# Kernel optimization log

Measured on AMD Instinct MI355X. Metric: run time of the kernel, lower is better.

Reference implementation:

```python
import jax, jax.numpy as jnp
import numpy as np

DIM = 2048
NUM_HEADS = 16
HEAD_DIM = 128
INNER = NUM_HEADS * HEAD_DIM


def rotate_half(x):
    x1, x2 = jnp.split(x, 2, axis=-1)
    return jnp.concatenate([-x2, x1], axis=-1)


def rope_tables(T, head_dim):
    inv_freq = 1.0 / (10000.0 ** (np.arange(0, head_dim, 2, dtype=np.float32) / head_dim))
    t = np.arange(T, dtype=np.float32)
    freqs = np.einsum('i,j->ij', t, inv_freq)  # [T, hd/2]
    emb = np.concatenate([freqs, freqs], axis=-1)  # [T, hd]
    return jnp.asarray(np.cos(emb)), jnp.asarray(np.sin(emb))


def setup_inputs() -> dict:
    key = jax.random.key(0)
    k1, k2, k3 = jax.random.split(key, 3)
    B, T = 2, 2048
    x = jax.random.normal(k1, (B, T, DIM), dtype=jnp.float32)
    scale = 1.0 / np.sqrt(DIM)
    w_qkv = jax.random.normal(k2, (DIM, 3 * INNER), dtype=jnp.float32) * scale
    w_out = jax.random.normal(k3, (INNER, DIM), dtype=jnp.float32) * (1.0 / np.sqrt(INNER))
    return {"x": x, "w_qkv": w_qkv, "w_out": w_out}


def reference(x, w_qkv, w_out):
    B, T, _ = x.shape
    qkv = x @ w_qkv  # [B, T, 3*INNER]
    q, k, v = jnp.split(qkv, 3, axis=-1)
    # [B, H, T, hd]
    q = q.reshape(B, T, NUM_HEADS, HEAD_DIM).transpose(0, 2, 1, 3)
    k = k.reshape(B, T, NUM_HEADS, HEAD_DIM).transpose(0, 2, 1, 3)
    v = v.reshape(B, T, NUM_HEADS, HEAD_DIM).transpose(0, 2, 1, 3)
    cos, sin = rope_tables(T, HEAD_DIM)  # [T, hd]
    cos = cos[None, None]
    sin = sin[None, None]
    q = q * cos + rotate_half(q) * sin
    k = k * cos + rotate_half(k) * sin
    # causal SDPA
    scale = 1.0 / np.sqrt(HEAD_DIM)
    scores = jnp.einsum('bhqd,bhkd->bhqk', q, k) * scale
    mask = jnp.tril(jnp.ones((T, T), dtype=bool))
    scores = jnp.where(mask[None, None], scores, jnp.finfo(scores.dtype).min)
    attn = jax.nn.softmax(scores, axis=-1)
    out = jnp.einsum('bhqk,bhkd->bhqd', attn, v)
    out = out.transpose(0, 2, 1, 3).reshape(B, T, INNER)
    return out @ w_out
```

## Files before the change

### kernel.cpp

```cpp
#include <hip/hip_runtime.h>
#include <hip/hip_bf16.h>
#include <math.h>

typedef __bf16 bf16x8 __attribute__((ext_vector_type(8)));
typedef float f32x4 __attribute__((ext_vector_type(4)));
typedef float f32x16 __attribute__((ext_vector_type(16)));
typedef unsigned short ushort8_t __attribute__((ext_vector_type(8)));
typedef unsigned short ushort4_t __attribute__((ext_vector_type(4)));

#define DIMSZ 2048
#define NHEADS 16
#define HD 128
#define INNER 2048
#define T_SEQ 2048
#define BATCH 2
#define BT_ROWS (BATCH * T_SEQ)
#define QKV_COLS (3 * INNER)

__device__ __forceinline__ float bf2f(unsigned short u) {
  union { unsigned int ui; float f; } v; v.ui = ((unsigned int)u) << 16; return v.f;
}
__device__ __forceinline__ unsigned short f2bf(float f) {
  union { float f; unsigned int ui; } v; v.f = f;
  unsigned int u = v.ui;
  return (unsigned short)((u + 0x7FFFu + ((u >> 16) & 1u)) >> 16);
}
__device__ __forceinline__ bf16x8 ld8(const unsigned short* p) {
  return *(const bf16x8*)p;
}
__device__ __forceinline__ void gl16(const unsigned short* g, unsigned short* l) {
  __builtin_amdgcn_global_load_lds(
      (const __attribute__((address_space(1))) unsigned int*)g,
      (__attribute__((address_space(3))) unsigned int*)l, 16, 0, 0);
}

__global__ void detect_dtype(const unsigned short* __restrict__ w, int* __restrict__ flag) {
  __shared__ int sh;
  if (threadIdx.x == 0) sh = 0;
  __syncthreads();
  int hit = 0;
  for (int i = threadIdx.x; i < 8192; i += 256) {
    unsigned int e = (w[i] >> 7) & 0xFF;
    if (e >= 0x7F) hit = 1;
  }
  if (hit) atomicOr(&sh, 1);
  __syncthreads();
  if (threadIdx.x == 0) *flag = sh;
}

__global__ void convert_x(const void* __restrict__ in, unsigned short* __restrict__ out,
                          const int* __restrict__ flag) {
  const bool f32 = (*flag != 0);
  size_t i = ((size_t)blockIdx.x * 256 + threadIdx.x) * 8;
  if (f32) {
    const float* inf = (const float*)in;
    float4 u0 = *(const float4*)&inf[i];
    float4 u1 = *(const float4*)&inf[i + 4];
    ushort8_t t;
    t[0] = f2bf(u0.x); t[1] = f2bf(u0.y); t[2] = f2bf(u0.z); t[3] = f2bf(u0.w);
    t[4] = f2bf(u1.x); t[5] = f2bf(u1.y); t[6] = f2bf(u1.z); t[7] = f2bf(u1.w);
    *(ushort8_t*)&out[i] = t;
  } else {
    *(uint4*)&out[i] = *(const uint4*)&((const unsigned short*)in)[i];
  }
}

__global__ void transpose_any(const void* __restrict__ in, unsigned short* __restrict__ out,
                              int R, int C, const int* __restrict__ flag) {
  const bool f32 = (*flag != 0);
  __shared__ unsigned short tile[32][33];
  int c0 = blockIdx.x * 32, r0 = blockIdx.y * 32;
  int tx = threadIdx.x & 31, ty = threadIdx.x >> 5;
  if (f32) {
    const float* inf = (const float*)in;
    #pragma unroll
    for (int i = 0; i < 4; ++i)
      tile[ty + i * 8][tx] = f2bf(inf[(size_t)(r0 + ty + i * 8) * C + c0 + tx]);
  } else {
    const unsigned short* inu = (const unsigned short*)in;
    #pragma unroll
    for (int i = 0; i < 4; ++i)
      tile[ty + i * 8][tx] = inu[(size_t)(r0 + ty + i * 8) * C + c0 + tx];
  }
  __syncthreads();
  #pragma unroll
  for (int i = 0; i < 4; ++i)
    out[(size_t)(c0 + ty + i * 8) * R + r0 + tx] = tile[tx][ty + i * 8];
}

__global__ __launch_bounds__(256) void gemm_lds(const unsigned short* __restrict__ A,
                                                const unsigned short* __restrict__ Bt,
                                                unsigned short* __restrict__ Cb,
                                                float* __restrict__ Cf,
                                                int M, int N, int K) {
  __shared__ unsigned short As[128 * 32];
  __shared__ unsigned short Bs[128 * 32];
  const int tid = threadIdx.x;
  const int m0 = blockIdx.y * 128, n0 = blockIdx.x * 128;
  const int w = tid >> 6, L = tid & 63, lane = tid & 63, c = lane & 15, quad = lane >> 4;
  const int wm = (w & 1) * 64, wn = (w >> 1) * 64;
  f32x4 acc[4][4];
  #pragma unroll
  for (int i = 0; i < 4; ++i)
    #pragma unroll
    for (int j = 0; j < 4; ++j) acc[i][j] = (f32x4)0.0f;

  for (int k0 = 0; k0 < K; k0 += 32) {
    #pragma unroll
    for (int p = 0; p < 2; ++p) {
      int ci = p * 256 + w * 64 + L;
      int r = ci >> 2, s = ci & 3;
      gl16(&A[(size_t)(m0 + r) * K + k0 + s * 8], &As[(size_t)(p * 256 + w * 64) * 8]);
      gl16(&Bt[(size_t)(n0 + r) * K + k0 + s * 8], &Bs[(size_t)(p * 256 + w * 64) * 8]);
    }
    __syncthreads();
    bf16x8 af[4], bfr[4];
    #pragma unroll
    for (int i = 0; i < 4; ++i) af[i] = ld8(&As[(wm + i * 16 + c) * 32 + quad * 8]);
    #pragma unroll
    for (int j = 0; j < 4; ++j) bfr[j] = ld8(&Bs[(wn + j * 16 + c) * 32 + quad * 8]);
    #pragma unroll
    for (int i = 0; i < 4; ++i)
      #pragma unroll
      for (int j = 0; j < 4; ++j)
        acc[i][j] = __builtin_amdgcn_mfma_f32_16x16x32_bf16(af[i], bfr[j], acc[i][j], 0, 0, 0);
    __syncthreads();
  }
  if (Cf) {
    #pragma unroll
    for (int i = 0; i < 4; ++i)
      #pragma unroll
      for (int j = 0; j < 4; ++j)
        #pragma unroll
        for (int r = 0; r < 4; ++r)
          Cf[(size_t)(m0 + wm + i * 16 + quad * 4 + r) * N + n0 + wn + j * 16 + c] = acc[i][j][r];
  } else {
    #pragma unroll
    for (int i = 0; i < 4; ++i)
      #pragma unroll
      for (int j = 0; j < 4; ++j)
        #pragma unroll
        for (int r = 0; r < 4; ++r)
          Cb[(size_t)(m0 + wm + i * 16 + quad * 4 + r) * N + n0 + wn + j * 16 + c] =
              f2bf(acc[i][j][r]);
  }
}

__global__ void rope_kernel(unsigned short* __restrict__ qkv) {
  int idx = blockIdx.x * 256 + threadIdx.x;
  int jb = (idx & 7) * 8;
  int head = (idx >> 3) & 15;
  int qk = (idx >> 7) & 1;
  int row = idx >> 8;
  int t = row & (T_SEQ - 1);
  size_t base = (size_t)row * QKV_COLS + qk * INNER + head * HD + jb;
  ushort8_t x1 = *(ushort8_t*)&qkv[base];
  ushort8_t x2 = *(ushort8_t*)&qkv[base + 64];
  ushort8_t o1, o2;
  #pragma unroll
  for (int e = 0; e < 8; ++e) {
    float inv_freq = exp2f(-(float)(jb + e) * 0.20762050593046017f);
    float ang = (float)t * inv_freq;
    float sn = sinf(ang), cs = cosf(ang);
    float a = bf2f(x1[e]), bq = bf2f(x2[e]);
    o1[e] = f2bf(a * cs - bq * sn);
    o2[e] = f2bf(bq * cs + a * sn);
  }
  *(ushort8_t*)&qkv[base] = o1;
  *(ushort8_t*)&qkv[base + 64] = o2;
}

#define KT3 64
#define KSTR3 136
#define VSTR3 72
#define PSTR3 68
#define SM_VS (64 * KSTR3 * 2)
#define SM_PS (SM_VS + 128 * VSTR3 * 2)
#define SM_LR (SM_PS + 64 * PSTR3 * 2)
#define SM_TOT (SM_LR + 2 * 64 * 4)
__global__ __launch_bounds__(256, 2) void flash_attn3(const unsigned short* __restrict__ qkv,
                                                      unsigned short* __restrict__ aout) {
  __shared__ char smem[SM_TOT];
  unsigned short* Ks = (unsigned short*)smem;
  unsigned short* Vs = (unsigned short*)(smem + SM_VS);
  unsigned short* Ps = (unsigned short*)(smem + SM_PS);
  float* lred = (float*)(smem + SM_LR);
  float* Os = (float*)smem;

  const int tid = threadIdx.x, wave = tid >> 6, lane = tid & 63;
  const int wq = wave & 1, wk = wave >> 1;
  const int l31 = lane & 31, lh = lane >> 5;
  const int bh = blockIdx.y, b = bh >> 4, h = bh & 15;
  const unsigned short* qbase = qkv + (size_t)b * T_SEQ * QKV_COLS + h * HD;
  const unsigned short* kbase = qbase + INNER;
  const unsigned short* vbase = qbase + 2 * INNER;
  const float cf = 0.12751743f;

  for (int half = 0; half < 2; ++half) {
    const int qt = (half == 0) ? (int)blockIdx.x : 31 - (int)blockIdx.x;
    const int q0 = qt * 64;
    const int qg = q0 + wq * 32 + l31;

    bf16x8 aq[8];
    #pragma unroll
    for (int ch = 0; ch < 8; ++ch)
      aq[ch] = ld8(&qbase[(size_t)qg * QKV_COLS + ch * 16 + lh * 8]);

    f32x16 o[4];
    #pragma unroll
    for (int dt = 0; dt < 4; ++dt) o[dt] = (f32x16)0.0f;
    float l_part = 0.0f;

    const int nkt = qt + 1;
    for (int it = 0; it < nkt; ++it) {
      const int kt = it * KT3;
      __syncthreads();
      #pragma unroll
      for (int p = 0; p < 4; ++p) {
        int ci = p * 256 + tid, r = ci >> 4, s = ci & 15;
        *(uint4*)&Ks[r * KSTR3 + s * 8] = *(const uint4*)&kbase[(size_t)(kt + r) * QKV_COLS + s * 8];
      }
      {
        int rp = tid & 31, seg = tid >> 5;
        const unsigned short* vp = &vbase[(size_t)(kt + 2 * rp) * QKV_COLS + seg * 16];
        ushort8_t v0a = *(const ushort8_t*)vp;
        ushort8_t v0b = *(const ushort8_t*)(vp + 8);
        ushort8_t v1a = *(const ushort8_t*)(vp + QKV_COLS);
        ushort8_t v1b = *(const ushort8_t*)(vp + QKV_COLS + 8);
        #pragma unroll
        for (int e = 0; e < 8; ++e) {
          *(unsigned int*)&Vs[(seg * 16 + e) * VSTR3 + 2 * rp] =
              (unsigned int)v0a[e] | ((unsigned int)v1a[e] << 16);
          *(unsigned int*)&Vs[(seg * 16 + 8 + e) * VSTR3 + 2 * rp] =
              (unsigned int)v0b[e] | ((unsigned int)v1b[e] << 16);
        }
      }
      __syncthreads();

      f32x16 st = (f32x16)0.0f;
      #pragma unroll
      for (int ch = 0; ch < 8; ++ch) {
        bf16x8 kf = ld8(&Ks[(wk * 32 + l31) * KSTR3 + ch * 16 + lh * 8]);
        st = __builtin_amdgcn_mfma_f32_32x32x16_bf16(kf, aq[ch], st, 0, 0, 0);
      }
      unsigned short* prow = &Ps[(wq * 32 + l31) * PSTR3 + wk * 32];
      #pragma unroll
      for (int g = 0; g < 4; ++g) {
        ushort4_t pk;
        #pragma unroll
        for (int e = 0; e < 4; ++e) {
          int r = g * 4 + e;
          int keyl = e + 8 * g + 4 * lh;
          int kg = kt + wk * 32 + keyl;
          float p = (kg <= qg) ? exp2f(st[r] * cf) : 0.0f;
          l_part += p;
          pk[e] = f2bf(p);
        }
        *(ushort4_t*)&prow[g * 8 + 4 * lh] = pk;
      }
      bf16x8 pf[2];
      #pragma unroll
      for (int kc = 0; kc < 2; ++kc) {
        uint2 pa = *(const uint2*)&Ps[(wq * 32 + l31) * PSTR3 + wk * 32 + kc * 16 + lh * 8];
        uint2 pb = *(const uint2*)&Ps[(wq * 32 + l31) * PSTR3 + wk * 32 + kc * 16 + lh * 8 + 4];
        union { uint4 u; bf16x8 v; } cvt;
        cvt.u.x = pa.x; cvt.u.y = pa.y; cvt.u.z = pb.x; cvt.u.w = pb.y;
        pf[kc] = cvt.v;
      }
      #pragma unroll
      for (int dt = 0; dt < 4; ++dt) {
        #pragma unroll
        for (int kc = 0; kc < 2; ++kc) {
          bf16x8 vf = ld8(&Vs[(dt * 32 + l31) * VSTR3 + wk * 32 + kc * 16 + lh * 8]);
          o[dt] = __builtin_amdgcn_mfma_f32_32x32x16_bf16(pf[kc], vf, o[dt], 0, 0, 0);
        }
      }
    }

    float lv = l_part + __shfl_xor(l_part, 32, 64);
    __syncthreads();
    if (lane < 32) lred[wk * 64 + wq * 32 + lane] = lv;
    if (wk == 1) {
      #pragma unroll
      for (int dt = 0; dt < 4; ++dt)
        #pragma unroll
        for (int s = 0; s < 4; ++s) {
          f32x4 seg4 = {o[dt][s * 4 + 0], o[dt][s * 4 + 1], o[dt][s * 4 + 2], o[dt][s * 4 + 3]};
          *(f32x4*)&Os[(size_t)(wq * 64 + lane) * 68 + dt * 16 + s * 4] = seg4;
        }
    }
    __syncthreads();
    if (wk == 0) {
      float invr[16];
      #pragma unroll
      for (int r = 0; r < 16; ++r) {
        int ql = wq * 32 + (r & 3) + 8 * (r >> 2) + 4 * lh;
        invr[r] = 1.0f / (lred[ql] + lred[64 + ql]);
      }
      #pragma unroll
      for (int dt = 0; dt < 4; ++dt) {
        f32x4 add[4];
        #pragma unroll
        for (int s = 0; s < 4; ++s)
          add[s] = *(const f32x4*)&Os[(size_t)(wq * 64 + lane) * 68 + dt * 16 + s * 4];
        #pragma unroll
        for (int r = 0; r < 16; ++r) {
          float val = (o[dt][r] + add[r >> 2][r & 3]) * invr[r];
          int qrow = q0 + wq * 32 + (r & 3) + 8 * (r >> 2) + 4 * lh;
          aout[(size_t)((size_t)b * T_SEQ + qrow) * INNER + h * HD + dt * 32 + l31] = f2bf(val);
        }
      }
    }
  }
}

extern "C" void kernel_launch(void* const* d_in, const int* in_sizes, int n_in,
                              void* d_out, int out_size, void* d_ws, size_t ws_size,
                              hipStream_t stream) {
  const void* x     = d_in[0];
  const void* w_qkv = d_in[1];
  const void* w_out = d_in[2];
  float* out = (float*)d_out;

  int* flag = (int*)d_ws;
  unsigned short* qkvbuf  = (unsigned short*)((char*)d_ws + 256);
  unsigned short* attnout = qkvbuf + (size_t)BT_ROWS * QKV_COLS;
  unsigned short* wqkvT   = attnout + (size_t)BT_ROWS * INNER;
  unsigned short* woutT   = wqkvT + (size_t)QKV_COLS * DIMSZ;
  unsigned short* xb      = woutT + (size_t)DIMSZ * INNER;

  detect_dtype<<<1, 256, 0, stream>>>((const unsigned short*)w_qkv, flag);
  convert_x<<<dim3((size_t)BT_ROWS * DIMSZ / 2048), 256, 0, stream>>>(x, xb, flag);
  transpose_any<<<dim3(QKV_COLS / 32, DIMSZ / 32), 256, 0, stream>>>(w_qkv, wqkvT, DIMSZ, QKV_COLS, flag);
  transpose_any<<<dim3(DIMSZ / 32, INNER / 32), 256, 0, stream>>>(w_out, woutT, INNER, DIMSZ, flag);
  gemm_lds<<<dim3(QKV_COLS / 128, BT_ROWS / 128), 256, 0, stream>>>(xb, wqkvT, qkvbuf, nullptr, BT_ROWS, QKV_COLS, DIMSZ);
  rope_kernel<<<dim3(BT_ROWS * NHEADS * 2 * 8 / 256), 256, 0, stream>>>(qkvbuf);
  flash_attn3<<<dim3(16, BATCH * NHEADS), 256, 0, stream>>>(qkvbuf, attnout);
  gemm_lds<<<dim3(DIMSZ / 128, BT_ROWS / 128), 256, 0, stream>>>(attnout, woutT, nullptr, out, BT_ROWS, DIMSZ, INNER);
}
```

Baseline: 451.6 us.

## Fuse RoPE into QKV GEMM epilogue, widen K tile with swizzle, prefetch KV

The QKV projection now applies rotary embedding in its epilogue, reading precomputed cos/sin tables that a small kernel fills once per call, so the separate rope kernel and its full read/write of Q and K are gone. The GEMM K-step is widened from 32 to 64 with an XOR-swizzled LDS layout to reduce bank conflicts and halve barrier count. The attention kernel now prefetches the next K/V tile into registers while the current tile is being computed. The costs are higher register and LDS use, and the tables are stored in the attention-output buffer, which is safe only because they are consumed before attention writes that buffer.

```diff
diff --git a/kernel.cpp b/kernel.cpp
--- a/kernel.cpp
+++ b/kernel.cpp
@@ -88,16 +88,33 @@
     out[(size_t)(c0 + ty + i * 8) * R + r0 + tx] = tile[tx][ty + i * 8];
 }
 
-__global__ __launch_bounds__(256) void gemm_lds(const unsigned short* __restrict__ A,
-                                                const unsigned short* __restrict__ Bt,
-                                                unsigned short* __restrict__ Cb,
-                                                float* __restrict__ Cf,
-                                                int M, int N, int K) {
-  __shared__ unsigned short As[128 * 32];
-  __shared__ unsigned short Bs[128 * 32];
+__global__ void rope_tables(float* __restrict__ ct, float* __restrict__ st) {
+  int i = blockIdx.x * 256 + threadIdx.x;
+  int t = i >> 6, j = i & 63;
+  float inv_freq = exp2f(-(float)j * 0.20762050593046017f);
+  float ang = (float)t * inv_freq;
+  ct[i] = cosf(ang);
+  st[i] = sinf(ang);
+}
+
+#define GBK 64
+__global__ __launch_bounds__(256) void gemm_lds2(const unsigned short* __restrict__ A,
+                                                 const unsigned short* __restrict__ Bt,
+                                                 unsigned short* __restrict__ Cb,
+                                                 float* __restrict__ Cf,
+                                                 int M, int N, int K,
+                                                 const float* __restrict__ costab,
+                                                 const float* __restrict__ sintab,
+                                                 int rope_limit) {
+  __shared__ union {
+    unsigned short stage[2][128 * GBK];
+    unsigned short tile[128 * 136];
+  } sm;
+  unsigned short* As = sm.stage[0];
+  unsigned short* Bs = sm.stage[1];
   const int tid = threadIdx.x;
   const int m0 = blockIdx.y * 128, n0 = blockIdx.x * 128;
-  const int w = tid >> 6, L = tid & 63, lane = tid & 63, c = lane & 15, quad = lane >> 4;
+  const int w = tid >> 6, L = tid & 63, c = L & 15, quad = L >> 4;
   const int wm = (w & 1) * 64, wn = (w >> 1) * 64;
   f32x4 acc[4][4];
   #pragma unroll
@@ -105,25 +122,31 @@
     #pragma unroll
     for (int j = 0; j < 4; ++j) acc[i][j] = (f32x4)0.0f;
 
-  for (int k0 = 0; k0 < K; k0 += 32) {
-    #pragma unroll
-    for (int p = 0; p < 2; ++p) {
+  for (int k0 = 0; k0 < K; k0 += GBK) {
+    #pragma unroll
+    for (int p = 0; p < 4; ++p) {
       int ci = p * 256 + w * 64 + L;
-      int r = ci >> 2, s = ci & 3;
-      gl16(&A[(size_t)(m0 + r) * K + k0 + s * 8], &As[(size_t)(p * 256 + w * 64) * 8]);
-      gl16(&Bt[(size_t)(n0 + r) * K + k0 + s * 8], &Bs[(size_t)(p * 256 + w * 64) * 8]);
-    }
-    __syncthreads();
-    bf16x8 af[4], bfr[4];
-    #pragma unroll
-    for (int i = 0; i < 4; ++i) af[i] = ld8(&As[(wm + i * 16 + c) * 32 + quad * 8]);
-    #pragma unroll
-    for (int j = 0; j < 4; ++j) bfr[j] = ld8(&Bs[(wn + j * 16 + c) * 32 + quad * 8]);
-    #pragma unroll
-    for (int i = 0; i < 4; ++i)
+      int r = ci >> 3, s = ci & 7;
+      int sl = s ^ (r & 7);
+      gl16(&A[(size_t)(m0 + r) * K + k0 + sl * 8], &As[(p * 256 + w * 64) * 8]);
+      gl16(&Bt[(size_t)(n0 + r) * K + k0 + sl * 8], &Bs[(p * 256 + w * 64) * 8]);
+    }
+    __syncthreads();
+    #pragma unroll
+    for (int sub = 0; sub < 2; ++sub) {
+      bf16x8 af[4], bfr[4];
+      #pragma unroll
+      for (int i = 0; i < 4; ++i)
+        af[i] = ld8(&As[(wm + i * 16 + c) * GBK + (((sub * 4 + quad) ^ (c & 7)) * 8)]);
       #pragma unroll
       for (int j = 0; j < 4; ++j)
-        acc[i][j] = __builtin_amdgcn_mfma_f32_16x16x32_bf16(af[i], bfr[j], acc[i][j], 0, 0, 0);
+        bfr[j] = ld8(&Bs[(wn + j * 16 + c) * GBK + (((sub * 4 + quad) ^ (c & 7)) * 8)]);
+      #pragma unroll
+      for (int i = 0; i < 4; ++i)
+        #pragma unroll
+        for (int j = 0; j < 4; ++j)
+          acc[i][j] = __builtin_amdgcn_mfma_f32_16x16x32_bf16(af[i], bfr[j], acc[i][j], 0, 0, 0);
+    }
     __syncthreads();
   }
   if (Cf) {
@@ -134,6 +157,40 @@
         #pragma unroll
         for (int r = 0; r < 4; ++r)
           Cf[(size_t)(m0 + wm + i * 16 + quad * 4 + r) * N + n0 + wn + j * 16 + c] = acc[i][j][r];
+  } else if (n0 < rope_limit) {
+    #pragma unroll
+    for (int i = 0; i < 4; ++i)
+      #pragma unroll
+      for (int j = 0; j < 4; ++j)
+        #pragma unroll
+        for (int r = 0; r < 4; ++r)
+          sm.tile[(wm + i * 16 + quad * 4 + r) * 136 + wn + j * 16 + c] = f2bf(acc[i][j][r]);
+    __syncthreads();
+    int rbase = w * 8 + (L >> 3);
+    int cb = (L & 7) * 8;
+    #pragma unroll
+    for (int p = 0; p < 4; ++p) {
+      int row = rbase + p * 32;
+      int tp = (m0 + row) & (T_SEQ - 1);
+      const float* cr = &costab[tp * 64 + cb];
+      const float* sr = &sintab[tp * 64 + cb];
+      float4 c0v = *(const float4*)cr, c1v = *(const float4*)(cr + 4);
+      float4 s0v = *(const float4*)sr, s1v = *(const float4*)(sr + 4);
+      float cv[8] = {c0v.x, c0v.y, c0v.z, c0v.w, c1v.x, c1v.y, c1v.z, c1v.w};
+      float sv[8] = {s0v.x, s0v.y, s0v.z, s0v.w, s1v.x, s1v.y, s1v.z, s1v.w};
+      bf16x8 x1 = ld8(&sm.tile[row * 136 + cb]);
+      bf16x8 x2 = ld8(&sm.tile[row * 136 + cb + 64]);
+      ushort8_t o1, o2;
+      #pragma unroll
+      for (int e = 0; e < 8; ++e) {
+        float a = (float)x1[e], bq = (float)x2[e];
+        o1[e] = f2bf(a * cv[e] - bq * sv[e]);
+        o2[e] = f2bf(bq * cv[e] + a * sv[e]);
+      }
+      *(ushort8_t*)&Cb[(size_t)(m0 + row) * N + n0 + cb] = o1;
+      *(ushort8_t*)&Cb[(size_t)(m0 + row) * N + n0 + cb + 64] = o2;
+    }
+    __syncthreads();
   } else {
     #pragma unroll
     for (int i = 0; i < 4; ++i)
@@ -144,30 +201,6 @@
           Cb[(size_t)(m0 + wm + i * 16 + quad * 4 + r) * N + n0 + wn + j * 16 + c] =
               f2bf(acc[i][j][r]);
   }
-}
-
-__global__ void rope_kernel(unsigned short* __restrict__ qkv) {
-  int idx = blockIdx.x * 256 + threadIdx.x;
-  int jb = (idx & 7) * 8;
-  int head = (idx >> 3) & 15;
-  int qk = (idx >> 7) & 1;
-  int row = idx >> 8;
-  int t = row & (T_SEQ - 1);
-  size_t base = (size_t)row * QKV_COLS + qk * INNER + head * HD + jb;
-  ushort8_t x1 = *(ushort8_t*)&qkv[base];
-  ushort8_t x2 = *(ushort8_t*)&qkv[base + 64];
-  ushort8_t o1, o2;
-  #pragma unroll
-  for (int e = 0; e < 8; ++e) {
-    float inv_freq = exp2f(-(float)(jb + e) * 0.20762050593046017f);
-    float ang = (float)t * inv_freq;
-    float sn = sinf(ang), cs = cosf(ang);
-    float a = bf2f(x1[e]), bq = bf2f(x2[e]);
-    o1[e] = f2bf(a * cs - bq * sn);
-    o2[e] = f2bf(bq * cs + a * sn);
-  }
-  *(ushort8_t*)&qkv[base] = o1;
-  *(ushort8_t*)&qkv[base + 64] = o2;
 }
 
 #define KT3 64
@@ -178,7 +211,7 @@
 #define SM_PS (SM_VS + 128 * VSTR3 * 2)
 #define SM_LR (SM_PS + 64 * PSTR3 * 2)
 #define SM_TOT (SM_LR + 2 * 64 * 4)
-__global__ __launch_bounds__(256, 2) void flash_attn3(const unsigned short* __restrict__ qkv,
+__global__ __launch_bounds__(256, 2) void flash_attn4(const unsigned short* __restrict__ qkv,
                                                       unsigned short* __restrict__ aout) {
   __shared__ char smem[SM_TOT];
   unsigned short* Ks = (unsigned short*)smem;
@@ -195,6 +228,22 @@
   const unsigned short* kbase = qbase + INNER;
   const unsigned short* vbase = qbase + 2 * INNER;
   const float cf = 0.12751743f;
+  const int rp = tid & 31, seg = tid >> 5;
+
+  uint4 kreg[4];
+  ushort8_t v0a, v0b, v1a, v1b;
+  auto loadKV = [&](int kt) {
+    #pragma unroll
+    for (int p = 0; p < 4; ++p) {
+      int ci = p * 256 + tid, r = ci >> 4, s = ci & 15;
+      kreg[p] = *(const uint4*)&kbase[(size_t)(kt + r) * QKV_COLS + s * 8];
+    }
+    const unsigned short* vp = &vbase[(size_t)(kt + 2 * rp) * QKV_COLS + seg * 16];
+    v0a = *(const ushort8_t*)vp;
+    v0b = *(const ushort8_t*)(vp + 8);
+    v1a = *(const ushort8_t*)(vp + QKV_COLS);
+    v1b = *(const ushort8_t*)(vp + QKV_COLS + 8);
+  };
 
   for (int half = 0; half < 2; ++half) {
     const int qt = (half == 0) ? (int)blockIdx.x : 31 - (int)blockIdx.x;
@@ -212,29 +261,22 @@
     float l_part = 0.0f;
 
     const int nkt = qt + 1;
+    loadKV(0);
     for (int it = 0; it < nkt; ++it) {
-      const int kt = it * KT3;
       __syncthreads();
       #pragma unroll
       for (int p = 0; p < 4; ++p) {
         int ci = p * 256 + tid, r = ci >> 4, s = ci & 15;
-        *(uint4*)&Ks[r * KSTR3 + s * 8] = *(const uint4*)&kbase[(size_t)(kt + r) * QKV_COLS + s * 8];
-      }
-      {
-        int rp = tid & 31, seg = tid >> 5;
-        const unsigned short* vp = &vbase[(size_t)(kt + 2 * rp) * QKV_COLS + seg * 16];
-        ushort8_t v0a = *(const ushort8_t*)vp;
-        ushort8_t v0b = *(const ushort8_t*)(vp + 8);
-        ushort8_t v1a = *(const ushort8_t*)(vp + QKV_COLS);
-        ushort8_t v1b = *(const ushort8_t*)(vp + QKV_COLS + 8);
-        #pragma unroll
-        for (int e = 0; e < 8; ++e) {
-          *(unsigned int*)&Vs[(seg * 16 + e) * VSTR3 + 2 * rp] =
-              (unsigned int)v0a[e] | ((unsigned int)v1a[e] << 16);
-          *(unsigned int*)&Vs[(seg * 16 + 8 + e) * VSTR3 + 2 * rp] =
-              (unsigned int)v0b[e] | ((unsigned int)v1b[e] << 16);
-        }
-      }
+        *(uint4*)&Ks[r * KSTR3 + s * 8] = kreg[p];
+      }
+      #pragma unroll
+      for (int e = 0; e < 8; ++e) {
+        *(unsigned int*)&Vs[(seg * 16 + e) * VSTR3 + 2 * rp] =
+            (unsigned int)v0a[e] | ((unsigned int)v1a[e] << 16);
+        *(unsigned int*)&Vs[(seg * 16 + 8 + e) * VSTR3 + 2 * rp] =
+            (unsigned int)v0b[e] | ((unsigned int)v1b[e] << 16);
+      }
+      if (it + 1 < nkt) loadKV((it + 1) * KT3);
       __syncthreads();
 
       f32x16 st = (f32x16)0.0f;
@@ -243,6 +285,7 @@
         bf16x8 kf = ld8(&Ks[(wk * 32 + l31) * KSTR3 + ch * 16 + lh * 8]);
         st = __builtin_amdgcn_mfma_f32_32x32x16_bf16(kf, aq[ch], st, 0, 0, 0);
       }
+      const int kt = it * KT3;
       unsigned short* prow = &Ps[(wq * 32 + l31) * PSTR3 + wk * 32];
       #pragma unroll
       for (int g = 0; g < 4; ++g) {
@@ -328,13 +371,17 @@
   unsigned short* wqkvT   = attnout + (size_t)BT_ROWS * INNER;
   unsigned short* woutT   = wqkvT + (size_t)QKV_COLS * DIMSZ;
   unsigned short* xb      = woutT + (size_t)DIMSZ * INNER;
+  float* costab = (float*)attnout;
+  float* sintab = costab + T_SEQ * 64;
 
   detect_dtype<<<1, 256, 0, stream>>>((const unsigned short*)w_qkv, flag);
   convert_x<<<dim3((size_t)BT_ROWS * DIMSZ / 2048), 256, 0, stream>>>(x, xb, flag);
   transpose_any<<<dim3(QKV_COLS / 32, DIMSZ / 32), 256, 0, stream>>>(w_qkv, wqkvT, DIMSZ, QKV_COLS, flag);
   transpose_any<<<dim3(DIMSZ / 32, INNER / 32), 256, 0, stream>>>(w_out, woutT, INNER, DIMSZ, flag);
-  gemm_lds<<<dim3(QKV_COLS / 128, BT_ROWS / 128), 256, 0, stream>>>(xb, wqkvT, qkvbuf, nullptr, BT_ROWS, QKV_COLS, DIMSZ);
-  rope_kernel<<<dim3(BT_ROWS * NHEADS * 2 * 8 / 256), 256, 0, stream>>>(qkvbuf);
-  flash_attn3<<<dim3(16, BATCH * NHEADS), 256, 0, stream>>>(qkvbuf, attnout);
-  gemm_lds<<<dim3(DIMSZ / 128, BT_ROWS / 128), 256, 0, stream>>>(attnout, woutT, nullptr, out, BT_ROWS, DIMSZ, INNER);
-}
+  rope_tables<<<dim3(T_SEQ * 64 / 256), 256, 0, stream>>>(costab, sintab);
+  gemm_lds2<<<dim3(QKV_COLS / 128, BT_ROWS / 128), 256, 0, stream>>>(
+      xb, wqkvT, qkvbuf, nullptr, BT_ROWS, QKV_COLS, DIMSZ, costab, sintab, 2 * INNER);
+  flash_attn4<<<dim3(16, BATCH * NHEADS), 256, 0, stream>>>(qkvbuf, attnout);
+  gemm_lds2<<<dim3(DIMSZ / 128, BT_ROWS / 128), 256, 0, stream>>>(
+      attnout, woutT, nullptr, out, BT_ROWS, DIMSZ, INNER, nullptr, nullptr, 0);
+}
```

Result: no change. 453.5 us (+0.4%).
